# Kernel tuning notes

Hardware: AMD Instinct MI355X
Metric: run time of the kernel (lower is better)

Reference implementation:

```python
import jax, jax.numpy as jnp
import numpy as np

B, NR, NF, NH, NFH, D, HID = 32, 32, 128, 64, 64, 32, 256


def setup_inputs() -> dict:
    key = jax.random.key(0)
    ks = jax.random.split(key, 16)

    def w(k, o, i):
        return (jax.random.normal(k, (o, i), jnp.float32) / np.sqrt(i)).astype(jnp.float32)

    inp = {
        "robot": jax.random.normal(ks[0], (B, NR, D), jnp.float32),
        "frontier": jax.random.normal(ks[1], (B, NF, D), jnp.float32),
        "robot_history": jax.random.normal(ks[2], (B, NH, D), jnp.float32),
        "frontier_history": jax.random.normal(ks[3], (B, NFH, D), jnp.float32),
        "robot_frontier": jax.random.uniform(ks[4], (B, NR, NF), jnp.float32),
        "robot_past": jax.random.uniform(ks[5], (B, NR, NH), jnp.float32),
        "frontier_past": jax.random.uniform(ks[6], (B, NF, NFH), jnp.float32),
        # parameters (torch Linear convention: weight [out, in])
        "Wq": w(ks[7], D, D), "bq": jnp.zeros(D, jnp.float32),
        "Wk": w(ks[8], D, D), "bk": jnp.zeros(D, jnp.float32),
        "Wv": w(ks[9], D, D), "bv": jnp.zeros(D, jnp.float32),
        "Wn1": w(ks[10], HID, 2 * D), "bn1": jnp.zeros(HID, jnp.float32),
        "Wn2": w(ks[11], D, HID), "bn2": jnp.zeros(D, jnp.float32),
        "We1": w(ks[12], HID, 2 * D + 1), "be1": jnp.zeros(HID, jnp.float32),
        "We2": w(ks[13], 1, HID), "be2": jnp.zeros(1, jnp.float32),
    }
    return inp


def reference(robot, frontier, robot_history, frontier_history, robot_frontier,
              robot_past, frontier_past, Wq, bq, Wk, bk, Wv, bv,
              Wn1, bn1, Wn2, bn2, We1, be1, We2, be2):
    def lin(x, W, b):
        return x @ W.T + b

    def nmlp(h):
        return lin(jax.nn.relu(lin(h, Wn1, bn1)), Wn2, bn2)

    def emlp(h):
        return lin(jax.nn.relu(lin(h, We1, be1)), We2, be2)

    def intra(x):  # x: [b, n, D]
        q, k, v = lin(x, Wq, bq), lin(x, Wk, bk), lin(x, Wv, bv)
        e = jax.nn.softmax(jnp.einsum('bnd,bmd->bnm', q, k), axis=-1)
        agg = jnp.einsum('bnm,bmd->bnd', e, v)
        return x + nmlp(jnp.concatenate([x, agg], axis=-1))

    def inter(x, y, dis):  # x: [b,Nx,D], y: [b,Ny,D], dis: [b,Nx,Ny]
        xq, yk, yv = lin(x, Wq, bq), lin(y, Wk, bk), lin(y, Wv, bv)
        b, Nx, _ = x.shape
        Ny = y.shape[1]
        r_i = jnp.broadcast_to(xq[:, :, None, :], (b, Nx, Ny, D))
        f_j = jnp.broadcast_to(yk[:, None, :, :], (b, Nx, Ny, D))
        edge_input = jnp.concatenate([r_i, f_j, dis[..., None]], axis=-1)  # [b,Nx,Ny,65]
        score = emlp(edge_input)[..., 0]                                   # [b,Nx,Ny]
        e = jax.nn.softmax(score, axis=-1)
        agg = jnp.einsum('bnm,bmd->bnd', e, yv)
        x = x + nmlp(jnp.concatenate([x, agg], axis=-1))
        return e, x

    robot = intra(robot)
    frontier = intra(frontier)           # == per-sample intra on [1,Nf,D]
    robot_history = intra(robot_history)
    frontier_history = intra(frontier_history)
    _, robot = inter(robot, robot_history, robot_past)
    _, new_frontier = inter(frontier, frontier_history, frontier_past)
    edge, robot = inter(robot, new_frontier, robot_frontier)
    # original returns the intra-transformed frontier (split_frontier), not new_frontier
    return (robot, frontier, robot_history, frontier_history, edge)
```

## Files before the change

### kernel.cpp

```cpp
#include <hip/hip_runtime.h>

#define BATCH 32
#define NRr 32
#define NFf 128
#define NHh 64
#define NFHh 64
#define TI 4

__device__ __forceinline__ float dot4(float4 a, float4 b) {
    return fmaf(a.x, b.x, fmaf(a.y, b.y, fmaf(a.z, b.z, a.w * b.w)));
}

__global__ __launch_bounds__(256) void intra_kernel(
    const float* __restrict__ robot, const float* __restrict__ frontier,
    const float* __restrict__ rhist, const float* __restrict__ fhist,
    const float* __restrict__ Wq, const float* __restrict__ bq,
    const float* __restrict__ Wk, const float* __restrict__ bk,
    const float* __restrict__ Wv, const float* __restrict__ bv,
    const float* __restrict__ Wn1, const float* __restrict__ bn1,
    const float* __restrict__ Wn2, const float* __restrict__ bn2,
    float* __restrict__ o_robot, float* __restrict__ o_frontier,
    float* __restrict__ o_rh, float* __restrict__ o_fh)
{
    __shared__ __align__(16) float sXc[1024];
    __shared__ __align__(16) float sQ[1024];
    __shared__ __align__(16) float sQK[1024];
    __shared__ __align__(16) float sAgg[1024];
    __shared__ __align__(16) float sBig[8448];
    float* sS  = sBig;
    float* sXT = sBig + 4224;
    float* sT  = sBig;

    const int blk = blockIdx.x, tid = threadIdx.x;
    const float* xin; float* xout; int N, lgN, b, chunk;
    if (blk < 32)       { xin=robot;    xout=o_robot;    N=32;  lgN=5; b=blk;          chunk=0; }
    else if (blk < 160) { xin=frontier; xout=o_frontier; N=128; lgN=7; b=(blk-32)>>2;  chunk=(blk-32)&3; }
    else if (blk < 224) { xin=rhist;    xout=o_rh;       N=64;  lgN=6; b=(blk-160)>>1; chunk=(blk-160)&1; }
    else                { xin=fhist;    xout=o_fh;       N=64;  lgN=6; b=(blk-224)>>1; chunk=(blk-224)&1; }

    const int P = N + 4, P2 = N + 1;
    const float* xb = xin + (size_t)b * N * 32;
    const int r0 = chunk << 5;
    const int d = tid & 31;

    {
        int idx = tid;
        #pragma unroll
        for (int it = 0; it < 4; ++it, idx += 256)
            sXc[idx] = xb[(r0 << 5) + idx];
    }
    for (int idx = tid; idx < (N << 5); idx += 256) {
        int j = idx >> 5, d2 = idx & 31;
        sXT[d2 * P2 + j] = xb[idx];
    }
    __syncthreads();

    {
        const float4* wq4 = (const float4*)(Wq + (d << 5));
        float4 wq[8];
        #pragma unroll
        for (int k = 0; k < 8; ++k) wq[k] = wq4[k];
        const float bqd = bq[d];
        int idx = tid;
        #pragma unroll
        for (int it = 0; it < 4; ++it, idx += 256) {
            int r = idx >> 5;
            const float4* xr = (const float4*)(sXc + (r << 5));
            float a = bqd;
            #pragma unroll
            for (int k = 0; k < 8; ++k) a += dot4(wq[k], xr[k]);
            sQ[idx] = a;
        }
    }
    __syncthreads();

    {
        int idx = tid;
        #pragma unroll
        for (int it = 0; it < 4; ++it, idx += 256) {
            int r = idx >> 5, e = idx & 31;
            const float* qr = sQ + (r << 5);
            float a = 0.f;
            #pragma unroll
            for (int dd2 = 0; dd2 < 32; ++dd2)
                a = fmaf(Wk[dd2 * 32 + e], qr[dd2], a);
            sQK[idx] = a;
        }
    }
    __syncthreads();

    for (int idx = tid; idx < (N << 5); idx += 256) {
        int r = idx >> lgN, j = idx & (N - 1);
        const float* qr = sQK + (r << 5);
        float a = 0.f;
        #pragma unroll
        for (int e = 0; e < 32; ++e) a = fmaf(qr[e], sXT[e * P2 + j], a);
        sS[r * P + j] = a;
    }
    __syncthreads();

    {
        int r = tid >> 3, l = tid & 7;
        float* row = sS + r * P;
        float m = -1e30f;
        for (int j = l; j < N; j += 8) m = fmaxf(m, row[j]);
        m = fmaxf(m, __shfl_xor(m, 4));
        m = fmaxf(m, __shfl_xor(m, 2));
        m = fmaxf(m, __shfl_xor(m, 1));
        float s = 0.f;
        for (int j = l; j < N; j += 8) { float ev = __expf(row[j] - m); row[j] = ev; s += ev; }
        s += __shfl_xor(s, 4); s += __shfl_xor(s, 2); s += __shfl_xor(s, 1);
        float inv = 1.0f / s;
        for (int j = l; j < N; j += 8) row[j] *= inv;
    }
    __syncthreads();

    {
        int idx = tid;
        #pragma unroll
        for (int it = 0; it < 4; ++it, idx += 256) {
            int r = idx >> 5, d2 = idx & 31;
            const float* er = sS + r * P;
            const float* xtr = sXT + d2 * P2;
            float a = 0.f;
            for (int j = 0; j < N; ++j) a = fmaf(er[j], xtr[j], a);
            sQ[idx] = a;
        }
    }
    __syncthreads();

    {
        const float4* wv4 = (const float4*)(Wv + (d << 5));
        float4 wv[8];
        #pragma unroll
        for (int k = 0; k < 8; ++k) wv[k] = wv4[k];
        const float bvd = bv[d];
        int idx = tid;
        #pragma unroll
        for (int it = 0; it < 4; ++it, idx += 256) {
            int r = idx >> 5;
            const float4* zr = (const float4*)(sQ + (r << 5));
            float a = bvd;
            #pragma unroll
            for (int k = 0; k < 8; ++k) a += dot4(wv[k], zr[k]);
            sAgg[idx] = a;
        }
    }
    __syncthreads();

    {
        const float4* w14 = (const float4*)(Wn1 + (tid << 6));
        float4 w1r[16];
        #pragma unroll
        for (int k = 0; k < 16; ++k) w1r[k] = w14[k];
        const float b1 = bn1[tid];
        for (int r = 0; r < 32; ++r) {
            const float4* xr = (const float4*)(sXc + (r << 5));
            const float4* ar = (const float4*)(sAgg + (r << 5));
            float a = b1;
            #pragma unroll
            for (int k = 0; k < 8; ++k) a += dot4(w1r[k], xr[k]);
            #pragma unroll
            for (int k = 0; k < 8; ++k) a += dot4(w1r[8 + k], ar[k]);
            sT[(r << 8) + tid] = fmaxf(a, 0.f);
        }
    }
    __syncthreads();

    {
        const int rg = tid >> 5;
        float acc[4] = {0.f, 0.f, 0.f, 0.f};
        #pragma unroll
        for (int hc = 0; hc < 4; ++hc) {
            const float4* w24 = (const float4*)(Wn2 + (d << 8) + (hc << 6));
            float4 w2r[16];
            #pragma unroll
            for (int k = 0; k < 16; ++k) w2r[k] = w24[k];
            #pragma unroll
            for (int p = 0; p < 4; ++p) {
                int r = rg + (p << 3);
                const float4* tr = (const float4*)(sT + (r << 8) + (hc << 6));
                float a = 0.f;
                #pragma unroll
                for (int k = 0; k < 16; ++k) a += dot4(w2r[k], tr[k]);
                acc[p] += a;
            }
        }
        const float b2 = bn2[d];
        #pragma unroll
        for (int p = 0; p < 4; ++p) {
            int r = rg + (p << 3);
            xout[((size_t)b * N << 5) + ((r0 + r) << 5) + d] = sXc[(r << 5) + d] + b2 + acc[p];
        }
    }
}

__global__ __launch_bounds__(256) void pre_y_kernel(
    const float* __restrict__ yA, int NyA, float* __restrict__ wOutA, float* __restrict__ yvOutA, int nBlkA,
    const float* __restrict__ yB, int NyB, float* __restrict__ wOutB, float* __restrict__ yvOutB,
    const float* __restrict__ Wk, const float* __restrict__ bk,
    const float* __restrict__ Wv, const float* __restrict__ bv,
    const float* __restrict__ We1)
{
    __shared__ __align__(16) float sY[256], sK[256];
    const int blk = blockIdx.x, tid = threadIdx.x;
    const float* y; int Ny; float* wOut; float* yvOut; int idx;
    if (blk < nBlkA) { y=yA; Ny=NyA; wOut=wOutA; yvOut=yvOutA; idx=blk; }
    else             { y=yB; Ny=NyB; wOut=wOutB; yvOut=yvOutB; idx=blk-nBlkA; }
    const int chunks = Ny >> 3;
    const int b = idx / chunks, j0 = (idx - b * chunks) << 3;

    sY[tid] = y[((size_t)(b * Ny + j0)) * 32 + tid];
    __syncthreads();

    {
        int jl = tid >> 5, dd = tid & 31;
        const float4* wk4 = (const float4*)(Wk + (dd << 5));
        const float4* wv4 = (const float4*)(Wv + (dd << 5));
        const float4* yr = (const float4*)(sY + (jl << 5));
        float aK = bk[dd], aV = bv[dd];
        #pragma unroll
        for (int k = 0; k < 8; ++k) {
            float4 yv4 = yr[k];
            aK += dot4(wk4[k], yv4);
            aV += dot4(wv4[k], yv4);
        }
        sK[(jl << 5) + dd] = aK;
        yvOut[((size_t)(b * Ny + j0 + jl)) * 32 + dd] = aV;
    }
    __syncthreads();

    {
        const float* w1 = We1 + tid * 65 + 32;
        float acc[8] = {0,0,0,0,0,0,0,0};
        #pragma unroll
        for (int e = 0; e < 32; ++e) {
            float we = w1[e];
            #pragma unroll
            for (int jl = 0; jl < 8; ++jl)
                acc[jl] = fmaf(we, sK[(jl << 5) + e], acc[jl]);
        }
        float* wbase = wOut + (((size_t)b * 64 + (tid >> 2)) * Ny + j0) * 4 + (tid & 3);
        #pragma unroll
        for (int jl = 0; jl < 8; ++jl)
            wbase[jl << 2] = acc[jl];
    }
}

__global__ __launch_bounds__(256) void inter_main_kernel(
    const float* __restrict__ xA, int NxA, const float* __restrict__ wA, const float* __restrict__ yvA,
    int NyA, const float* __restrict__ disA, float* __restrict__ outA, float* __restrict__ eA,
    float* __restrict__ wPreA, float* __restrict__ yvPreA, int nBlkA,
    const float* __restrict__ xB, int NxB, const float* __restrict__ wB, const float* __restrict__ yvB,
    int NyB, const float* __restrict__ disB, float* __restrict__ outB, float* __restrict__ eB,
    float* __restrict__ wPreB, float* __restrict__ yvPreB,
    const float* __restrict__ Wq, const float* __restrict__ bq,
    const float* __restrict__ Wk, const float* __restrict__ bk,
    const float* __restrict__ Wv, const float* __restrict__ bv,
    const float* __restrict__ We1, const float* __restrict__ be1,
    const float* __restrict__ We2,
    const float* __restrict__ Wn1, const float* __restrict__ bn1,
    const float* __restrict__ Wn2, const float* __restrict__ bn2)
{
    __shared__ __align__(16) float sX[128];
    __shared__ __align__(16) float sQ[128];
    __shared__ __align__(16) float sAgg[128];
    __shared__ __align__(16) float sDis[512];
    __shared__ __align__(16) float sC[256];
    __shared__ __align__(16) float sW2[256];
    __shared__ __align__(16) float sS[512];
    __shared__ __align__(16) float sUT[1024];
    __shared__ __align__(16) float sPR[2048];
    __shared__ __align__(16) float sYV[4096];

    const int blk = blockIdx.x, tid = threadIdx.x;
    const float* x; int Nx; const float* w; const float* yv; int Ny;
    const float* dis; float* outp; float* ep; float* wPre; float* yvPre; int idx;
    if (blk < nBlkA) { x=xA; Nx=NxA; w=wA; yv=yvA; Ny=NyA; dis=disA; outp=outA; ep=eA; wPre=wPreA; yvPre=yvPreA; idx=blk; }
    else             { x=xB; Nx=NxB; w=wB; yv=yvB; Ny=NyB; dis=disB; outp=outB; ep=eB; wPre=wPreB; yvPre=yvPreB; idx=blk-nBlkA; }
    const int lgNy = (Ny == 128) ? 7 : 6;
    const int tiles = Nx >> 2;
    const int b = idx / tiles, i0 = (idx - b * tiles) << 2;
    const float* xrow = x + ((size_t)(b * Nx + i0)) * 32;

    if (tid < 128) sX[tid] = xrow[tid];
    if (tid < Ny) {
        int il = tid >> (lgNy - 2), jq = tid & ((Ny >> 2) - 1);
        ((float4*)sDis)[(il << 5) + jq] =
            ((const float4*)(dis + ((size_t)(b * Nx + i0 + il)) * Ny))[jq];
    }
    {
        const float4* yv4 = (const float4*)(yv + ((size_t)(b * Ny) << 5));
        for (int k = tid; k < (Ny << 3); k += 256)
            ((float4*)sYV)[k] = yv4[k];
    }
    __syncthreads();

    if (tid < 128) {
        int il = tid >> 5, dd = tid & 31;
        const float4* wq4 = (const float4*)(Wq + (dd << 5));
        const float4* xr = (const float4*)(sX + (il << 5));
        float a = bq[dd];
        #pragma unroll
        for (int k = 0; k < 8; ++k) a += dot4(wq4[k], xr[k]);
        sQ[tid] = a;
    }
    __syncthreads();

    {
        const float* w1 = We1 + tid * 65;
        const float b1 = be1[tid];
        float acc[TI];
        #pragma unroll
        for (int il = 0; il < TI; ++il) acc[il] = b1;
        #pragma unroll
        for (int e = 0; e < 32; ++e) {
            float we = w1[e];
            #pragma unroll
            for (int il = 0; il < TI; ++il)
                acc[il] = fmaf(we, sQ[(il << 5) + e], acc[il]);
        }
        #pragma unroll
        for (int il = 0; il < TI; ++il) sUT[(il << 8) + tid] = acc[il];
        sC[tid] = w1[64];
        sW2[tid] = We2[tid];
    }
    __syncthreads();

    const int wv = tid >> 6, lane = tid & 63;
    {
        const int hc0 = wv << 4;
        const float4* wT4 = (const float4*)w + (size_t)(b * 64) * Ny;
        const float4* c4p = (const float4*)sC;
        const float4* p4p = (const float4*)sW2;
        if (Ny == 64) {
            float dv[TI];
            #pragma unroll
            for (int il = 0; il < TI; ++il) dv[il] = sDis[(il << 7) + lane];
            float acc[TI] = {0.f, 0.f, 0.f, 0.f};
            #pragma unroll
            for (int t = 0; t < 16; ++t) {
                int hc = hc0 + t;
                float4 w4 = wT4[((size_t)hc << 6) + lane];
                float4 c4 = c4p[hc], p4 = p4p[hc];
                #pragma unroll
                for (int il = 0; il < TI; ++il) {
                    float4 u4 = ((const float4*)(sUT + (il << 8)))[hc];
                    acc[il] = fmaf(p4.x, fmaxf(fmaf(c4.x, dv[il], u4.x + w4.x), 0.f), acc[il]);
                    acc[il] = fmaf(p4.y, fmaxf(fmaf(c4.y, dv[il], u4.y + w4.y), 0.f), acc[il]);
                    acc[il] = fmaf(p4.z, fmaxf(fmaf(c4.z, dv[il], u4.z + w4.z), 0.f), acc[il]);
                    acc[il] = fmaf(p4.w, fmaxf(fmaf(c4.w, dv[il], u4.w + w4.w), 0.f), acc[il]);
                }
            }
            #pragma unroll
            for (int il = 0; il < TI; ++il)
                sPR[(wv << 9) + (il << 7) + lane] = acc[il];
        } else {
            float dv0[TI], dv1[TI];
            #pragma unroll
            for (int il = 0; il < TI; ++il) {
                dv0[il] = sDis[(il << 7) + lane];
                dv1[il] = sDis[(il << 7) + 64 + lane];
            }
            float acc0[TI] = {0.f, 0.f, 0.f, 0.f};
            float acc1[TI] = {0.f, 0.f, 0.f, 0.f};
            #pragma unroll
            for (int t = 0; t < 16; ++t) {
                int hc = hc0 + t;
                float4 wa = wT4[((size_t)hc << 7) + lane];
                float4 wb = wT4[((size_t)hc << 7) + 64 + lane];
                float4 c4 = c4p[hc], p4 = p4p[hc];
                #pragma unroll
                for (int il = 0; il < TI; ++il) {
                    float4 u4 = ((const float4*)(sUT + (il << 8)))[hc];
                    acc0[il] = fmaf(p4.x, fmaxf(fmaf(c4.x, dv0[il], u4.x + wa.x), 0.f), acc0[il]);
                    acc0[il] = fmaf(p4.y, fmaxf(fmaf(c4.y, dv0[il], u4.y + wa.y), 0.f), acc0[il]);
                    acc0[il] = fmaf(p4.z, fmaxf(fmaf(c4.z, dv0[il], u4.z + wa.z), 0.f), acc0[il]);
                    acc0[il] = fmaf(p4.w, fmaxf(fmaf(c4.w, dv0[il], u4.w + wa.w), 0.f), acc0[il]);
                    acc1[il] = fmaf(p4.x, fmaxf(fmaf(c4.x, dv1[il], u4.x + wb.x), 0.f), acc1[il]);
                    acc1[il] = fmaf(p4.y, fmaxf(fmaf(c4.y, dv1[il], u4.y + wb.y), 0.f), acc1[il]);
                    acc1[il] = fmaf(p4.z, fmaxf(fmaf(c4.z, dv1[il], u4.z + wb.z), 0.f), acc1[il]);
                    acc1[il] = fmaf(p4.w, fmaxf(fmaf(c4.w, dv1[il], u4.w + wb.w), 0.f), acc1[il]);
                }
            }
            #pragma unroll
            for (int il = 0; il < TI; ++il) {
                sPR[(wv << 9) + (il << 7) + lane] = acc0[il];
                sPR[(wv << 9) + (il << 7) + 64 + lane] = acc1[il];
            }
        }
    }
    __syncthreads();

    for (int k = tid; k < (TI << lgNy); k += 256) {
        int il = k >> lgNy, j = k & (Ny - 1);
        int o = (il << 7) + j;
        sS[o] = sPR[o] + sPR[512 + o] + sPR[1024 + o] + sPR[1536 + o];
    }
    __syncthreads();

    {
        float v0 = sS[(wv << 7) + lane];
        float v1 = (Ny == 128) ? sS[(wv << 7) + 64 + lane] : -1e30f;
        float m = fmaxf(v0, v1);
        #pragma unroll
        for (int msk = 32; msk; msk >>= 1) m = fmaxf(m, __shfl_xor(m, msk));
        float e0 = __expf(v0 - m);
        float e1 = (Ny == 128) ? __expf(v1 - m) : 0.f;
        float s = e0 + e1;
        #pragma unroll
        for (int msk = 32; msk; msk >>= 1) s += __shfl_xor(s, msk);
        float inv = 1.0f / s;
        e0 *= inv; e1 *= inv;
        sS[(wv << 7) + lane] = e0;
        if (Ny == 128) sS[(wv << 7) + 64 + lane] = e1;
        if (ep) {
            float* erow = ep + ((size_t)(b * Nx + i0 + wv)) * Ny;
            erow[lane] = e0;
            if (Ny == 128) erow[64 + lane] = e1;
        }
    }

    {
        const int dd = lane & 31, jg = lane >> 5;
        float p = 0.f;
        for (int j = jg; j < Ny; j += 2)
            p = fmaf(sS[(wv << 7) + j], sYV[(j << 5) + dd], p);
        p += __shfl_xor(p, 32);
        if (jg == 0) sAgg[(wv << 5) + dd] = p;
    }
    __syncthreads();

    {
        const float4* w14 = (const float4*)(Wn1 + (tid << 6));
        const float b1 = bn1[tid];
        float acc[TI];
        #pragma unroll
        for (int il = 0; il < TI; ++il) acc[il] = b1;
        #pragma unroll
        for (int k = 0; k < 8; ++k) {
            float4 wa = w14[k];
            #pragma unroll
            for (int il = 0; il < TI; ++il)
                acc[il] += dot4(wa, ((const float4*)(sX + (il << 5)))[k]);
        }
        #pragma unroll
        for (int k = 0; k < 8; ++k) {
            float4 wb = w14[8 + k];
            #pragma unroll
            for (int il = 0; il < TI; ++il)
                acc[il] += dot4(wb, ((const float4*)(sAgg + (il << 5)))[k]);
        }
        __syncthreads();
        #pragma unroll
        for (int il = 0; il < TI; ++il) sUT[(il << 8) + tid] = fmaxf(acc[il], 0.f);
    }
    __syncthreads();

    {
        const int hg = tid >> 5, dd = tid & 31;
        const float4* w24 = (const float4*)(Wn2 + (dd << 8) + (hg << 5));
        float4 w2r[8];
        #pragma unroll
        for (int k = 0; k < 8; ++k) w2r[k] = w24[k];
        float p[TI] = {0.f, 0.f, 0.f, 0.f};
        #pragma unroll
        for (int k = 0; k < 8; ++k) {
            #pragma unroll
            for (int il = 0; il < TI; ++il)
                p[il] += dot4(w2r[k], ((const float4*)(sUT + (il << 8) + (hg << 5)))[k]);
        }
        #pragma unroll
        for (int il = 0; il < TI; ++il) sPR[(hg << 7) + (il << 5) + dd] = p[il];
    }
    __syncthreads();
    if (tid < 128) {
        int il = tid >> 5, dd = tid & 31;
        float a = bn2[dd] + sX[tid];
        #pragma unroll
        for (int hg = 0; hg < 8; ++hg) a += sPR[(hg << 7) + tid];
        outp[((size_t)(b * Nx + i0 + il)) * 32 + dd] = a;
        if (wPre) sQ[tid] = a;
    }

    if (wPre) {
        __syncthreads();
        {
            int t = tid & 127, il = t >> 5, dd = t & 31;
            const float4* wm4 = (const float4*)(((tid < 128) ? Wk : Wv) + (dd << 5));
            const float4* orow = (const float4*)(sQ + (il << 5));
            float a = (tid < 128) ? bk[dd] : bv[dd];
            #pragma unroll
            for (int k = 0; k < 8; ++k) a += dot4(wm4[k], orow[k]);
            if (tid < 128) sS[il * 33 + dd] = a;
            else yvPre[(((size_t)(b * Nx + i0 + il)) << 5) + dd] = a;
        }
        __syncthreads();
        {
            const float* w1 = We1 + tid * 65 + 32;
            float acc[4] = {0.f, 0.f, 0.f, 0.f};
            #pragma unroll
            for (int e = 0; e < 32; ++e) {
                float we = w1[e];
                #pragma unroll
                for (int il = 0; il < 4; ++il)
                    acc[il] = fmaf(we, sS[il * 33 + e], acc[il]);
            }
            float* wbase = wPre + (((size_t)b * 64 + (tid >> 2)) * Nx + i0) * 4 + (tid & 3);
            #pragma unroll
            for (int il = 0; il < 4; ++il)
                wbase[il << 2] = acc[il];
        }
    }
}

extern "C" void kernel_launch(void* const* d_in, const int* in_sizes, int n_in,
                              void* d_out, int out_size, void* d_ws, size_t ws_size,
                              hipStream_t stream) {
    const float* robot          = (const float*)d_in[0];
    const float* frontier       = (const float*)d_in[1];
    const float* rh             = (const float*)d_in[2];
    const float* fh             = (const float*)d_in[3];
    const float* robot_frontier = (const float*)d_in[4];
    const float* robot_past     = (const float*)d_in[5];
    const float* frontier_past  = (const float*)d_in[6];
    const float* Wq  = (const float*)d_in[7];  const float* bq  = (const float*)d_in[8];
    const float* Wk  = (const float*)d_in[9];  const float* bk  = (const float*)d_in[10];
    const float* Wv  = (const float*)d_in[11]; const float* bv  = (const float*)d_in[12];
    const float* Wn1 = (const float*)d_in[13]; const float* bn1 = (const float*)d_in[14];
    const float* Wn2 = (const float*)d_in[15]; const float* bn2 = (const float*)d_in[16];
    const float* We1 = (const float*)d_in[17]; const float* be1 = (const float*)d_in[18];
    const float* We2 = (const float*)d_in[19];

    float* out = (float*)d_out;
    float* out_robot    = out;
    float* out_frontier = out + 32768;
    float* out_rh       = out + 163840;
    float* out_fh       = out + 229376;
    float* out_edge     = out + 294912;

    float* W = (float*)d_ws;
    float* robot1 = W;
    float* robot2 = W + 32768;
    float* nf     = W + 65536;
    float* w5     = W + 196608;
    float* yv5    = W + 720896;
    float* w6     = W + 786432;
    float* yv6    = W + 1310720;
    float* w7     = W + 1376256;
    float* yv7    = W + 2424832;

    intra_kernel<<<288, 256, 0, stream>>>(robot, frontier, rh, fh,
        Wq, bq, Wk, bk, Wv, bv, Wn1, bn1, Wn2, bn2,
        robot1, out_frontier, out_rh, out_fh);

    pre_y_kernel<<<512, 256, 0, stream>>>(
        out_rh, NHh, w5, yv5, BATCH * NHh / 8,
        out_fh, NFHh, w6, yv6,
        Wk, bk, Wv, bv, We1);

    inter_main_kernel<<<1280, 256, 0, stream>>>(
        robot1, NRr, w5, yv5, NHh, robot_past, robot2,
        (float*)nullptr, (float*)nullptr, (float*)nullptr, BATCH * (NRr / TI),
        out_frontier, NFf, w6, yv6, NFHh, frontier_past, nf,
        (float*)nullptr, w7, yv7,
        Wq, bq, Wk, bk, Wv, bv, We1, be1, We2, Wn1, bn1, Wn2, bn2);

    inter_main_kernel<<<256, 256, 0, stream>>>(
        robot2, NRr, w7, yv7, NFf, robot_frontier, out_robot, out_edge,
        (float*)nullptr, (float*)nullptr, BATCH * (NRr / TI),
        robot2, NRr, w7, yv7, NFf, robot_frontier, out_robot, out_edge,
        (float*)nullptr, (float*)nullptr,
        Wq, bq, Wk, bk, Wv, bv, We1, be1, We2, Wn1, bn1, Wn2, bn2);
}
```

Measured before the change: 204.0 us.

## Fold Wq/Wk projections into We1 via precomputed combined weight matrices

Extra blocks in pre_y_kernel precompute G = We1[:, :32]·Wq and H = We1[:, 32:64]·Wk, plus the matching folded bias vectors. inter_main_kernel then computes the edge-MLP query term straight from x with G, skipping the separate Q projection and one barrier. The prepass builds the next stage's key term with H, dropping another projection and barrier. It also fuses the four-way partial-score reduction into the softmax read, removing a shared-memory pass and a sync. The cost is 32 extra blocks and a slightly different float rounding order.

```diff
diff --git a/kernel.cpp b/kernel.cpp
--- a/kernel.cpp
+++ b/kernel.cpp
@@ -198,12 +198,42 @@
 __global__ __launch_bounds__(256) void pre_y_kernel(
     const float* __restrict__ yA, int NyA, float* __restrict__ wOutA, float* __restrict__ yvOutA, int nBlkA,
     const float* __restrict__ yB, int NyB, float* __restrict__ wOutB, float* __restrict__ yvOutB,
+    int ghBase,
+    const float* __restrict__ Wq, const float* __restrict__ bq,
     const float* __restrict__ Wk, const float* __restrict__ bk,
     const float* __restrict__ Wv, const float* __restrict__ bv,
-    const float* __restrict__ We1)
+    const float* __restrict__ We1, const float* __restrict__ be1,
+    float* __restrict__ Gm, float* __restrict__ gvec,
+    float* __restrict__ Hm, float* __restrict__ hbvec)
 {
     __shared__ __align__(16) float sY[256], sK[256];
     const int blk = blockIdx.x, tid = threadIdx.x;
+
+    if (blk >= ghBase) {
+        const int hr = ((blk - ghBase) << 3) + (tid >> 5), e = tid & 31;
+        const float* w1q = We1 + hr * 65;
+        const float* w1k = w1q + 32;
+        float aG = 0.f, aH = 0.f;
+        #pragma unroll
+        for (int d2 = 0; d2 < 32; ++d2) {
+            aG = fmaf(w1q[d2], Wq[d2 * 32 + e], aG);
+            aH = fmaf(w1k[d2], Wk[d2 * 32 + e], aH);
+        }
+        Gm[(hr << 5) + e] = aG;
+        Hm[(hr << 5) + e] = aH;
+        if (e == 0) {
+            float ag = be1[hr], ahb = 0.f;
+            #pragma unroll
+            for (int d2 = 0; d2 < 32; ++d2) {
+                ag  = fmaf(w1q[d2], bq[d2], ag);
+                ahb = fmaf(w1k[d2], bk[d2], ahb);
+            }
+            gvec[hr] = ag;
+            hbvec[hr] = ahb;
+        }
+        return;
+    }
+
     const float* y; int Ny; float* wOut; float* yvOut; int idx;
     if (blk < nBlkA) { y=yA; Ny=NyA; wOut=wOutA; yvOut=yvOutA; idx=blk; }
     else             { y=yB; Ny=NyB; wOut=wOutB; yvOut=yvOutB; idx=blk-nBlkA; }
@@ -254,11 +284,10 @@
     const float* __restrict__ xB, int NxB, const float* __restrict__ wB, const float* __restrict__ yvB,
     int NyB, const float* __restrict__ disB, float* __restrict__ outB, float* __restrict__ eB,
     float* __restrict__ wPreB, float* __restrict__ yvPreB,
-    const float* __restrict__ Wq, const float* __restrict__ bq,
-    const float* __restrict__ Wk, const float* __restrict__ bk,
+    const float* __restrict__ Gm, const float* __restrict__ gvec,
+    const float* __restrict__ Hm, const float* __restrict__ hbvec,
     const float* __restrict__ Wv, const float* __restrict__ bv,
-    const float* __restrict__ We1, const float* __restrict__ be1,
-    const float* __restrict__ We2,
+    const float* __restrict__ We1, const float* __restrict__ We2,
     const float* __restrict__ Wn1, const float* __restrict__ bn1,
     const float* __restrict__ Wn2, const float* __restrict__ bn2)
 {
@@ -296,33 +325,22 @@
     }
     __syncthreads();
 
-    if (tid < 128) {
-        int il = tid >> 5, dd = tid & 31;
-        const float4* wq4 = (const float4*)(Wq + (dd << 5));
-        const float4* xr = (const float4*)(sX + (il << 5));
-        float a = bq[dd];
-        #pragma unroll
-        for (int k = 0; k < 8; ++k) a += dot4(wq4[k], xr[k]);
-        sQ[tid] = a;
-    }
-    __syncthreads();
-
-    {
-        const float* w1 = We1 + tid * 65;
-        const float b1 = be1[tid];
+    {
+        const float* grow = Gm + (tid << 5);
+        const float g0 = gvec[tid];
         float acc[TI];
         #pragma unroll
-        for (int il = 0; il < TI; ++il) acc[il] = b1;
+        for (int il = 0; il < TI; ++il) acc[il] = g0;
         #pragma unroll
         for (int e = 0; e < 32; ++e) {
-            float we = w1[e];
+            float we = grow[e];
             #pragma unroll
             for (int il = 0; il < TI; ++il)
-                acc[il] = fmaf(we, sQ[(il << 5) + e], acc[il]);
+                acc[il] = fmaf(we, sX[(il << 5) + e], acc[il]);
         }
         #pragma unroll
         for (int il = 0; il < TI; ++il) sUT[(il << 8) + tid] = acc[il];
-        sC[tid] = w1[64];
+        sC[tid] = We1[tid * 65 + 64];
         sW2[tid] = We2[tid];
     }
     __syncthreads();
@@ -392,16 +410,14 @@
     }
     __syncthreads();
 
-    for (int k = tid; k < (TI << lgNy); k += 256) {
-        int il = k >> lgNy, j = k & (Ny - 1);
-        int o = (il << 7) + j;
-        sS[o] = sPR[o] + sPR[512 + o] + sPR[1024 + o] + sPR[1536 + o];
-    }
-    __syncthreads();
-
-    {
-        float v0 = sS[(wv << 7) + lane];
-        float v1 = (Ny == 128) ? sS[(wv << 7) + 64 + lane] : -1e30f;
+    {
+        const int base = (wv << 7) + lane;
+        float v0 = sPR[base] + sPR[512 + base] + sPR[1024 + base] + sPR[1536 + base];
+        float v1 = -1e30f;
+        if (Ny == 128) {
+            const int b2 = base + 64;
+            v1 = sPR[b2] + sPR[512 + b2] + sPR[1024 + b2] + sPR[1536 + b2];
+        }
         float m = fmaxf(v0, v1);
         #pragma unroll
         for (int msk = 32; msk; msk >>= 1) m = fmaxf(m, __shfl_xor(m, msk));
@@ -412,8 +428,8 @@
         for (int msk = 32; msk; msk >>= 1) s += __shfl_xor(s, msk);
         float inv = 1.0f / s;
         e0 *= inv; e1 *= inv;
-        sS[(wv << 7) + lane] = e0;
-        if (Ny == 128) sS[(wv << 7) + 64 + lane] = e1;
+        sS[base] = e0;
+        if (Ny == 128) sS[base + 64] = e1;
         if (ep) {
             float* erow = ep + ((size_t)(b * Nx + i0 + wv)) * Ny;
             erow[lane] = e0;
@@ -485,26 +501,27 @@
 
     if (wPre) {
         __syncthreads();
+        if (tid < 128) {
+            int il = tid >> 5, dd = tid & 31;
+            const float4* wm4 = (const float4*)(Wv + (dd << 5));
+            const float4* orow = (const float4*)(sQ + (il << 5));
+            float a = bv[dd];
+            #pragma unroll
+            for (int k = 0; k < 8; ++k) a += dot4(wm4[k], orow[k]);
+            yvPre[(((size_t)(b * Nx + i0 + il)) << 5) + dd] = a;
+        }
         {
-            int t = tid & 127, il = t >> 5, dd = t & 31;
-            const float4* wm4 = (const float4*)(((tid < 128) ? Wk : Wv) + (dd << 5));
-            const float4* orow = (const float4*)(sQ + (il << 5));
-            float a = (tid < 128) ? bk[dd] : bv[dd];
-            #pragma unroll
-            for (int k = 0; k < 8; ++k) a += dot4(wm4[k], orow[k]);
-            if (tid < 128) sS[il * 33 + dd] = a;
-            else yvPre[(((size_t)(b * Nx + i0 + il)) << 5) + dd] = a;
-        }
-        __syncthreads();
-        {
-            const float* w1 = We1 + tid * 65 + 32;
-            float acc[4] = {0.f, 0.f, 0.f, 0.f};
+            const float* hrow = Hm + (tid << 5);
+            const float hb0 = hbvec[tid];
+            float acc[4];
+            #pragma unroll
+            for (int il = 0; il < 4; ++il) acc[il] = hb0;
             #pragma unroll
             for (int e = 0; e < 32; ++e) {
-                float we = w1[e];
+                float we = hrow[e];
                 #pragma unroll
                 for (int il = 0; il < 4; ++il)
-                    acc[il] = fmaf(we, sS[il * 33 + e], acc[il]);
+                    acc[il] = fmaf(we, sQ[(il << 5) + e], acc[il]);
             }
             float* wbase = wPre + (((size_t)b * 64 + (tid >> 2)) * Nx + i0) * 4 + (tid & 3);
             #pragma unroll
@@ -549,27 +566,33 @@
     float* yv6    = W + 1310720;
     float* w7     = W + 1376256;
     float* yv7    = W + 2424832;
+    float* Gm     = W + 2555904;
+    float* gvec   = W + 2564096;
+    float* Hm     = W + 2564352;
+    float* hbvec  = W + 2572544;
 
     intra_kernel<<<288, 256, 0, stream>>>(robot, frontier, rh, fh,
         Wq, bq, Wk, bk, Wv, bv, Wn1, bn1, Wn2, bn2,
         robot1, out_frontier, out_rh, out_fh);
 
-    pre_y_kernel<<<512, 256, 0, stream>>>(
+    pre_y_kernel<<<544, 256, 0, stream>>>(
         out_rh, NHh, w5, yv5, BATCH * NHh / 8,
         out_fh, NFHh, w6, yv6,
-        Wk, bk, Wv, bv, We1);
+        512,
+        Wq, bq, Wk, bk, Wv, bv, We1, be1,
+        Gm, gvec, Hm, hbvec);
 
     inter_main_kernel<<<1280, 256, 0, stream>>>(
         robot1, NRr, w5, yv5, NHh, robot_past, robot2,
         (float*)nullptr, (float*)nullptr, (float*)nullptr, BATCH * (NRr / TI),
         out_frontier, NFf, w6, yv6, NFHh, frontier_past, nf,
         (float*)nullptr, w7, yv7,
-        Wq, bq, Wk, bk, Wv, bv, We1, be1, We2, Wn1, bn1, Wn2, bn2);
+        Gm, gvec, Hm, hbvec, Wv, bv, We1, We2, Wn1, bn1, Wn2, bn2);
 
     inter_main_kernel<<<256, 256, 0, stream>>>(
         robot2, NRr, w7, yv7, NFf, robot_frontier, out_robot, out_edge,
         (float*)nullptr, (float*)nullptr, BATCH * (NRr / TI),
         robot2, NRr, w7, yv7, NFf, robot_frontier, out_robot, out_edge,
         (float*)nullptr, (float*)nullptr,
-        Wq, bq, Wk, bk, Wv, bv, We1, be1, We2, Wn1, bn1, Wn2, bn2);
+        Gm, gvec, Hm, hbvec, Wv, bv, We1, We2, Wn1, bn1, Wn2, bn2);
 }
```

Result: faster. 197.7 us (median of 2 runs) (-3.1%).
